# Kernel optimization log

Hardware: AMD Instinct MI355X
Metric: run time of the kernel (lower is better)

Reference implementation:

```python
import jax, jax.numpy as jnp
import numpy as np

B, S, D, H, FF, R = 4, 1024, 1024, 16, 4096, 128
DH = D // H


def rmsnorm(x, w, eps=1e-6):
    # matches torch: norm = ||x||_2 / sqrt(d); out = w * x / (norm + eps)
    n = jnp.sqrt(jnp.sum(x * x, axis=-1, keepdims=True)) / np.sqrt(x.shape[-1]).astype(np.float32)
    return w * x / (n + eps)


def setup_inputs() -> dict:
    key = jax.random.key(0)
    ks = jax.random.split(key, 20)
    def w(k, shape, s=0.02):
        return (jax.random.normal(k, shape, jnp.float32) * s)
    return {
        "x": jax.random.normal(ks[0], (B, S, D), jnp.float32),
        "norm1_w": jnp.ones((D,), jnp.float32),
        "Wq": w(ks[1], (D, D)), "bq": jnp.zeros((D,), jnp.float32),
        "Wk": w(ks[2], (D, D)), "bk": jnp.zeros((D,), jnp.float32),
        "Wv": w(ks[3], (D, D)), "bv": jnp.zeros((D,), jnp.float32),
        "Wz": w(ks[4], (D, D)), "bz": jnp.zeros((D,), jnp.float32),
        "Wg": w(ks[5], (D, D)), "bg": jnp.zeros((D,), jnp.float32),
        "gdw": w(ks[6], (R, D)), "gdb": jnp.zeros((R,), jnp.float32),
        "guw": w(ks[7], (D, R)), "gub": jnp.zeros((D,), jnp.float32),
        "Wo": w(ks[8], (D, D)), "bo": jnp.zeros((D,), jnp.float32),
        "norm2_w": jnp.ones((D,), jnp.float32),
        "f1w": w(ks[9], (FF, D)), "f1b": jnp.zeros((FF,), jnp.float32),
        "f2w": w(ks[10], (D, FF)), "f2b": jnp.zeros((D,), jnp.float32),
    }


def reference(x, norm1_w, Wq, bq, Wk, bk, Wv, bv, Wz, bz, Wg, bg,
              gdw, gdb, guw, gub, Wo, bo, norm2_w, f1w, f1b, f2w, f2b):
    b, s, d = x.shape
    h = d // DH
    # 1. Norm + Q/K/V/Z projections
    xn = rmsnorm(x, norm1_w)
    q = xn @ Wq.T + bq
    k = xn @ Wk.T + bk
    v = xn @ Wv.T + bv
    z = xn @ Wz.T + bz
    # 2-3. DPG decay: gamma_t = clamp(sigmoid(W_up ReLU(W_down z_t)))
    gamma = jax.nn.sigmoid(jax.nn.relu(z @ gdw.T + gdb) @ guw.T + gub)
    gamma = jnp.clip(gamma, 1e-6, 1.0 - 1e-6)
    # 4. Core recurrence: h_t = z_t * sigmoid(W_g h_{t-1}) + gamma_t * h_{t-1}
    def step(hprev, zg):
        zt, gt = zg
        hn = zt * jax.nn.sigmoid(hprev @ Wg.T + bg) + gt * hprev
        return hn, hn
    h0 = jnp.zeros((b, d), x.dtype)
    _, hs = jax.lax.scan(step, h0, (jnp.swapaxes(z, 0, 1), jnp.swapaxes(gamma, 0, 1)))
    hseq = jnp.swapaxes(hs, 0, 1)  # [B,S,D]
    # 5. Multi-head attention over Q,K,V
    qh = q.reshape(b, s, h, DH)
    kh = k.reshape(b, s, h, DH)
    vh = v.reshape(b, s, h, DH)
    scores = jnp.einsum('bqhd,bkhd->bhqk', qh, kh) / np.sqrt(DH).astype(np.float32)
    attn = jax.nn.softmax(scores, axis=-1)
    ao = jnp.einsum('bhqk,bkhd->bqhd', attn, vh).reshape(b, s, d)
    ao = ao @ Wo.T + bo
    # 6. Residuals
    y = x + ao + hseq
    # 7. FFN + output
    yn = rmsnorm(y, norm2_w)
    ff = jax.nn.gelu(yn @ f1w.T + f1b) @ f2w.T + f2b
    return y + ff
```

## Files before the change

### kernel.cpp

```cpp
#include <hip/hip_runtime.h>
#include <stdint.h>

#define DD 1024
#define SS 1024
#define NBS 32

typedef __attribute__((ext_vector_type(8))) __bf16 bf16x8;
typedef __attribute__((ext_vector_type(4))) float f32x4;

union Frag { uint4 u; bf16x8 b; };

__device__ __forceinline__ float bf2f(ushort u){ union{uint32_t i; float f;} c; c.i = ((uint32_t)u)<<16; return c.f; }
__device__ __forceinline__ float bflo(uint32_t p){ union{uint32_t i; float f;} c; c.i = p<<16; return c.f; }
__device__ __forceinline__ float bfhi(uint32_t p){ union{uint32_t i; float f;} c; c.i = p & 0xffff0000u; return c.f; }
__device__ __forceinline__ ushort f2bf(float f){
  union{float f; uint32_t u;} c; c.f = f;
  uint32_t u = c.u;
  return (ushort)((u + 0x7fffu + ((u>>16)&1u)) >> 16);
}

__global__ __launch_bounds__(256) void cast_k(const float* __restrict__ s,
    ushort* __restrict__ d, int n)
{
  int i = (blockIdx.x*256 + threadIdx.x)*4;
  if (i >= n) return;
  float4 v = *(const float4*)(s+i);
  ushort4 o; o.x=f2bf(v.x); o.y=f2bf(v.y); o.z=f2bf(v.z); o.w=f2bf(v.w);
  *(ushort4*)(d+i) = o;
}

__global__ __launch_bounds__(256) void rmsnorm_k(const float* __restrict__ X,
    const float* __restrict__ w, ushort* __restrict__ out)
{
  const int row = blockIdx.x, t = threadIdx.x;
  const float* x = X + (size_t)row*DD;
  float xs[4]; float s = 0.f;
  #pragma unroll
  for (int i=0;i<4;i++){ float v = x[t + i*256]; xs[i]=v; s += v*v; }
  #pragma unroll
  for (int off=32; off>0; off>>=1) s += __shfl_xor(s, off, 64);
  __shared__ float sred[4];
  if ((t&63)==0) sred[t>>6] = s;
  __syncthreads();
  s = sred[0]+sred[1]+sred[2]+sred[3];
  float inv = 1.f/(sqrtf(s)*0.03125f + 1e-6f);
  #pragma unroll
  for (int i=0;i<4;i++){
    int c2 = t + i*256;
    out[(size_t)row*DD + c2] = f2bf(xs[i]*inv*w[c2]);
  }
}

enum { ACT_NONE=0, ACT_RELU=1, ACT_SIG=2, ACT_GELU=3 };
enum { EPI_B16=0, EPI_DUAL=1, EPI_F32=2, EPI_Y=3, EPI_OUT=4 };

template<int ACT, int EPI>
__global__ __launch_bounds__(256) void gemm_bt(
    const ushort* __restrict__ A, const ushort* __restrict__ W,
    const float* __restrict__ bias, int N, int K,
    ushort* __restrict__ Ob, float* __restrict__ Of,
    const float* __restrict__ X32, const ushort* __restrict__ H16,
    const float* __restrict__ Yf)
{
  __shared__ __align__(16) ushort At[128*32];
  __shared__ __align__(16) ushort Wt[128*32];
  const int tid = threadIdx.x;
  const int wave = tid >> 6, lane = tid & 63;
  const int quad = lane >> 4, l16 = lane & 15;
  const int wr = wave >> 1, wc = wave & 1;
  const int m0 = blockIdx.x * 128, n0 = blockIdx.y * 128;

  f32x4 acc[4][4];
  const f32x4 vz = {0.f,0.f,0.f,0.f};
  #pragma unroll
  for (int i=0;i<4;i++)
    #pragma unroll
    for (int j=0;j<4;j++) acc[i][j] = vz;

  const ushort* gA = A + (size_t)(m0 + wave*32 + (lane>>2))*K + (lane&3)*8;
  const ushort* gW = W + (size_t)(n0 + wave*32 + (lane>>2))*K + (lane&3)*8;
  ushort* lA = At + wave*1024 + lane*8;
  ushort* lW = Wt + wave*1024 + lane*8;

  for (int ko = 0; ko < K; ko += 32) {
    uint4 va  = *(const uint4*)(gA + ko);
    uint4 va2 = *(const uint4*)(gA + ko + (size_t)16*K);
    uint4 vw  = *(const uint4*)(gW + ko);
    uint4 vw2 = *(const uint4*)(gW + ko + (size_t)16*K);
    __syncthreads();
    *(uint4*)lA          = va;
    *(uint4*)(lA + 512)  = va2;
    *(uint4*)lW          = vw;
    *(uint4*)(lW + 512)  = vw2;
    __syncthreads();
    Frag af[4], bfr[4];
    #pragma unroll
    for (int mi=0;mi<4;mi++)
      af[mi].u = *(const uint4*)&At[(wr*64 + mi*16 + l16)*32 + quad*8];
    #pragma unroll
    for (int ni=0;ni<4;ni++)
      bfr[ni].u = *(const uint4*)&Wt[(wc*64 + ni*16 + l16)*32 + quad*8];
    #pragma unroll
    for (int mi=0;mi<4;mi++)
      #pragma unroll
      for (int ni=0;ni<4;ni++)
        acc[mi][ni] = __builtin_amdgcn_mfma_f32_16x16x32_bf16(af[mi].b, bfr[ni].b, acc[mi][ni], 0,0,0);
  }

  float bia[4];
  #pragma unroll
  for (int ni=0;ni<4;ni++) bia[ni] = bias[n0 + wc*64 + ni*16 + l16];
  #pragma unroll
  for (int mi=0;mi<4;mi++) {
    const int row0 = m0 + wr*64 + mi*16 + quad*4;
    #pragma unroll
    for (int ni=0;ni<4;ni++) {
      const int col = n0 + wc*64 + ni*16 + l16;
      #pragma unroll
      for (int r=0;r<4;r++) {
        float vx = acc[mi][ni][r] + bia[ni];
        if (ACT == ACT_RELU) vx = fmaxf(vx, 0.f);
        else if (ACT == ACT_SIG) {
          vx = 1.f/(1.f+__expf(-vx));
          vx = fminf(fmaxf(vx, 1e-6f), 1.f-1e-6f);
        } else if (ACT == ACT_GELU) {
          float ci = 0.7978845608028654f*(vx + 0.044715f*vx*vx*vx);
          float th = 1.f - 2.f/(1.f + __expf(2.f*ci));
          vx = 0.5f*vx*(1.f+th);
        }
        size_t idx = (size_t)(row0 + r)*N + col;
        if (EPI == EPI_B16)      Ob[idx] = f2bf(vx);
        else if (EPI == EPI_DUAL){ Ob[idx] = f2bf(vx); Of[idx] = vx; }
        else if (EPI == EPI_F32)  Of[idx] = vx;
        else if (EPI == EPI_Y)    Of[idx] = vx + X32[idx] + bf2f(H16[idx]);
        else                      Of[idx] = vx + Yf[idx];
      }
    }
  }
}

__global__ __launch_bounds__(256) void attn_k(const ushort* __restrict__ q,
  const ushort* __restrict__ k, const ushort* __restrict__ v, ushort* __restrict__ ao)
{
  __shared__ __align__(16) ushort Ks[64*64];
  __shared__ __align__(16) ushort Vs[64*64];
  __shared__ float Ps[64*65];
  const int qt = blockIdx.x, bh = blockIdx.y;
  const int b = bh >> 4, h = bh & 15;
  const int t = threadIdx.x, r = t >> 2, seg = t & 3;
  const ushort* qrow = q + ((size_t)(b*SS + qt*64 + r))*DD + h*64;
  float qr[64];
  #pragma unroll
  for (int i=0;i<64;i+=8){
    uint4 u = *(const uint4*)(qrow + i);
    qr[i+0]=bflo(u.x); qr[i+1]=bfhi(u.x); qr[i+2]=bflo(u.y); qr[i+3]=bfhi(u.y);
    qr[i+4]=bflo(u.z); qr[i+5]=bfhi(u.z); qr[i+6]=bflo(u.w); qr[i+7]=bfhi(u.w);
  }
  float o[16];
  #pragma unroll
  for (int i=0;i<16;i++) o[i]=0.f;
  float mrun = -1e30f, lrun = 0.f;
  const int jrow = t >> 3, jch = t & 7;
  for (int kt=0; kt<16; kt++) {
    __syncthreads();
    const ushort* kg = k + ((size_t)(b*SS + kt*64))*DD + h*64;
    const ushort* vg = v + ((size_t)(b*SS + kt*64))*DD + h*64;
    #pragma unroll
    for (int part=0; part<2; part++){
      int j = jrow + part*32;
      *(uint4*)&Ks[j*64 + jch*8] = *(const uint4*)(kg + (size_t)j*DD + jch*8);
      *(uint4*)&Vs[j*64 + jch*8] = *(const uint4*)(vg + (size_t)j*DD + jch*8);
    }
    __syncthreads();
    float sc[16];
    #pragma unroll
    for (int jj=0;jj<16;jj++){
      int j = seg*16 + jj;
      float s_ = 0.f;
      #pragma unroll
      for (int i=0;i<64;i+=8){
        uint4 u = *(const uint4*)&Ks[j*64+i];
        s_ = fmaf(qr[i+0], bflo(u.x), s_); s_ = fmaf(qr[i+1], bfhi(u.x), s_);
        s_ = fmaf(qr[i+2], bflo(u.y), s_); s_ = fmaf(qr[i+3], bfhi(u.y), s_);
        s_ = fmaf(qr[i+4], bflo(u.z), s_); s_ = fmaf(qr[i+5], bfhi(u.z), s_);
        s_ = fmaf(qr[i+6], bflo(u.w), s_); s_ = fmaf(qr[i+7], bfhi(u.w), s_);
      }
      sc[jj] = s_ * 0.125f;
    }
    float mx = sc[0];
    #pragma unroll
    for (int jj=1;jj<16;jj++) mx = fmaxf(mx, sc[jj]);
    mx = fmaxf(mx, __shfl_xor(mx, 1, 64));
    mx = fmaxf(mx, __shfl_xor(mx, 2, 64));
    float mnew = fmaxf(mrun, mx);
    float psum = 0.f;
    #pragma unroll
    for (int jj=0;jj<16;jj++){
      float p = __expf(sc[jj]-mnew);
      Ps[r*65 + seg*16 + jj] = p;
      psum += p;
    }
    psum += __shfl_xor(psum, 1, 64);
    psum += __shfl_xor(psum, 2, 64);
    float alpha = __expf(mrun - mnew);
    lrun = lrun*alpha + psum;
    mrun = mnew;
    #pragma unroll
    for (int i=0;i<16;i++) o[i] *= alpha;
    __syncthreads();
    #pragma unroll 4
    for (int j=0;j<64;j++){
      float pj = Ps[r*65 + j];
      uint4 u0 = *(const uint4*)&Vs[j*64 + seg*16];
      uint4 u1 = *(const uint4*)&Vs[j*64 + seg*16 + 8];
      o[ 0]=fmaf(pj,bflo(u0.x),o[ 0]); o[ 1]=fmaf(pj,bfhi(u0.x),o[ 1]);
      o[ 2]=fmaf(pj,bflo(u0.y),o[ 2]); o[ 3]=fmaf(pj,bfhi(u0.y),o[ 3]);
      o[ 4]=fmaf(pj,bflo(u0.z),o[ 4]); o[ 5]=fmaf(pj,bfhi(u0.z),o[ 5]);
      o[ 6]=fmaf(pj,bflo(u0.w),o[ 6]); o[ 7]=fmaf(pj,bfhi(u0.w),o[ 7]);
      o[ 8]=fmaf(pj,bflo(u1.x),o[ 8]); o[ 9]=fmaf(pj,bfhi(u1.x),o[ 9]);
      o[10]=fmaf(pj,bflo(u1.y),o[10]); o[11]=fmaf(pj,bfhi(u1.y),o[11]);
      o[12]=fmaf(pj,bflo(u1.z),o[12]); o[13]=fmaf(pj,bfhi(u1.z),o[13]);
      o[14]=fmaf(pj,bflo(u1.w),o[14]); o[15]=fmaf(pj,bfhi(u1.w),o[15]);
    }
  }
  float invl = 1.f/lrun;
  ushort* orow = ao + ((size_t)(b*SS + qt*64 + r))*DD + h*64 + seg*16;
  #pragma unroll
  for (int i=0;i<16;i++) orow[i] = f2bf(o[i]*invl);
}

__global__ __launch_bounds__(256) void scan_k(
    const ushort* __restrict__ Wgb, const float* __restrict__ bg,
    const float* __restrict__ z32, const float* __restrict__ gm32,
    ushort* __restrict__ hseq, ushort* __restrict__ hstate)
{
  const int blk = blockIdx.x, t = threadIdx.x;
  const int wave = t>>6, lane = t&63, quad = lane>>4, c = lane&15;
  const int mt = wave & 1, kh = wave >> 1;
  const int nbase = blk*32 + mt*16;
  const bool epi = (kh == 0) && (c < 4);
  const int n0w = nbase + quad*4;
  Frag a[16];
  {
    const ushort* wrow = Wgb + (size_t)(nbase + c)*DD + kh*512 + quad*8;
    #pragma unroll
    for (int kt=0;kt<16;kt++) a[kt].u = *(const uint4*)(wrow + kt*32);
  }
  float bgv[4];
  #pragma unroll
  for (int r=0;r<4;r++) bgv[r] = bg[nbase + quad*4 + r];
  __shared__ __align__(16) ushort Hs[4096];
  __shared__ float redbuf[2][64][5];
  const int qi = (c*1024 + n0w) >> 2;
  int gmax = 256;

  float4 znx = {0,0,0,0}, gnx = {0,0,0,0};
  if (epi) {
    znx = *(const float4*)(z32  + ((size_t)c*SS + 0)*DD + n0w);
    gnx = *(const float4*)(gm32 + ((size_t)c*SS + 0)*DD + n0w);
  }

  for (int st=0; st<SS; st++) {
    if (st > 0) {
      const uint64_t* hrd = (const uint64_t*)(hstate + ((st+3)&3)*4096);
      uint64_t v0,v1,v2,v3;
      int guard = 0;
      for (;;) {
        v0 = __hip_atomic_load(hrd + t*4 + 0, __ATOMIC_RELAXED, __HIP_MEMORY_SCOPE_AGENT);
        v1 = __hip_atomic_load(hrd + t*4 + 1, __ATOMIC_RELAXED, __HIP_MEMORY_SCOPE_AGENT);
        v2 = __hip_atomic_load(hrd + t*4 + 2, __ATOMIC_RELAXED, __HIP_MEMORY_SCOPE_AGENT);
        v3 = __hip_atomic_load(hrd + t*4 + 3, __ATOMIC_RELAXED, __HIP_MEMORY_SCOPE_AGENT);
        bool ok = ((uint32_t)v0 != 0xFFFFFFFFu) & ((uint32_t)(v0>>32) != 0xFFFFFFFFu)
                & ((uint32_t)v1 != 0xFFFFFFFFu) & ((uint32_t)(v1>>32) != 0xFFFFFFFFu)
                & ((uint32_t)v2 != 0xFFFFFFFFu) & ((uint32_t)(v2>>32) != 0xFFFFFFFFu)
                & ((uint32_t)v3 != 0xFFFFFFFFu) & ((uint32_t)(v3>>32) != 0xFFFFFFFFu);
        if (ok) break;
        if (++guard > gmax) { gmax = 0; break; }
        __builtin_amdgcn_s_sleep(1);
      }
      if (epi) {
        uint64_t* rst = (uint64_t*)(hstate + ((st+2)&3)*4096);
        __hip_atomic_store(rst + qi, 0xFFFFFFFFFFFFFFFFull,
                           __ATOMIC_RELAXED, __HIP_MEMORY_SCOPE_AGENT);
      }
      uint64_t* hsd = (uint64_t*)Hs;
      hsd[t*4+0]=v0; hsd[t*4+1]=v1; hsd[t*4+2]=v2; hsd[t*4+3]=v3;
    }
    float4 zc = znx, gc = gnx;
    if (epi && (st+1 < SS)) {
      znx = *(const float4*)(z32  + ((size_t)c*SS + (st+1))*DD + n0w);
      gnx = *(const float4*)(gm32 + ((size_t)c*SS + (st+1))*DD + n0w);
    }
    if (st > 0) {
      asm volatile("s_waitcnt lgkmcnt(0)\ns_barrier" ::: "memory");
    }
    f32x4 acc = {0.f,0.f,0.f,0.f};
    if (st > 0) {
      f32x4 acc1 = {0.f,0.f,0.f,0.f};
      const uint4 z4 = make_uint4(0u,0u,0u,0u);
      #pragma unroll
      for (int kt=0;kt<16;kt+=2) {
        Frag b0, b1;
        b0.u = (c<4) ? *(const uint4*)&Hs[c*1024 + kh*512 + (kt  )*32 + quad*8] : z4;
        b1.u = (c<4) ? *(const uint4*)&Hs[c*1024 + kh*512 + (kt+1)*32 + quad*8] : z4;
        acc  = __builtin_amdgcn_mfma_f32_16x16x32_bf16(a[kt  ].b, b0.b, acc,  0,0,0);
        acc1 = __builtin_amdgcn_mfma_f32_16x16x32_bf16(a[kt+1].b, b1.b, acc1, 0,0,0);
      }
      #pragma unroll
      for (int r=0;r<4;r++) acc[r] += acc1[r];
    }
    if (kh == 1) {
      #pragma unroll
      for (int r=0;r<4;r++) redbuf[mt][lane][r] = acc[r];
    }
    asm volatile("s_waitcnt lgkmcnt(0)\ns_barrier" ::: "memory");
    if (epi) {
      ushort hb[4];
      float zr[4] = {zc.x, zc.y, zc.z, zc.w};
      float gr[4] = {gc.x, gc.y, gc.z, gc.w};
      #pragma unroll
      for (int r=0;r<4;r++) {
        float g = acc[r] + redbuf[mt][lane][r] + bgv[r];
        g = 1.f/(1.f+__expf(-g));
        float hp = (st>0) ? bf2f(Hs[c*1024 + n0w + r]) : 0.f;
        hb[r] = f2bf(zr[r]*g + gr[r]*hp);
      }
      uint32_t p0 = (uint32_t)hb[0] | ((uint32_t)hb[1]<<16);
      uint32_t p1 = (uint32_t)hb[2] | ((uint32_t)hb[3]<<16);
      uint64_t pk = ((uint64_t)p1<<32) | (uint64_t)p0;
      uint64_t* hwd = (uint64_t*)(hstate + (st&3)*4096);
      __hip_atomic_store(hwd + qi, pk, __ATOMIC_RELAXED, __HIP_MEMORY_SCOPE_AGENT);
      uint2* sq = (uint2*)(hseq + ((size_t)c*SS + st)*DD + n0w);
      *sq = make_uint2(p0, p1);
    }
    asm volatile("s_waitcnt lgkmcnt(0)\ns_barrier" ::: "memory");
  }
}

extern "C" void kernel_launch(void* const* d_in, const int* in_sizes, int n_in,
                              void* d_out, int out_size, void* d_ws, size_t ws_size,
                              hipStream_t stream)
{
  const float* x   = (const float*)d_in[0];
  const float* n1w = (const float*)d_in[1];
  const float* Wq  = (const float*)d_in[2];
  const float* bq  = (const float*)d_in[3];
  const float* Wk  = (const float*)d_in[4];
  const float* bk  = (const float*)d_in[5];
  const float* Wv  = (const float*)d_in[6];
  const float* bv  = (const float*)d_in[7];
  const float* Wz  = (const float*)d_in[8];
  const float* bz  = (const float*)d_in[9];
  const float* Wg_ = (const float*)d_in[10];
  const float* bg  = (const float*)d_in[11];
  const float* gdw = (const float*)d_in[12];
  const float* gdb = (const float*)d_in[13];
  const float* guw = (const float*)d_in[14];
  const float* gub = (const float*)d_in[15];
  const float* Wo  = (const float*)d_in[16];
  const float* bo  = (const float*)d_in[17];
  const float* n2w = (const float*)d_in[18];
  const float* f1w = (const float*)d_in[19];
  const float* f1b = (const float*)d_in[20];
  const float* f2w = (const float*)d_in[21];
  const float* f2b = (const float*)d_in[22];

  char* ws = (char*)d_ws;
  const size_t MB = (size_t)1<<20;
  ushort* Wqb  = (ushort*)(ws +  0*MB);
  ushort* Wkb  = (ushort*)(ws +  2*MB);
  ushort* Wvb  = (ushort*)(ws +  4*MB);
  ushort* Wzb  = (ushort*)(ws +  6*MB);
  ushort* Wob  = (ushort*)(ws +  8*MB);
  ushort* Wgb  = (ushort*)(ws + 10*MB);
  ushort* gdwb = (ushort*)(ws + 12*MB);
  ushort* guwb = (ushort*)(ws + 12*MB + (512<<10));
  ushort* f1wb = (ushort*)(ws + 13*MB);
  ushort* f2wb = (ushort*)(ws + 21*MB);
  ushort* xn   = (ushort*)(ws + 29*MB);
  ushort* qb   = (ushort*)(ws + 37*MB);
  ushort* kb   = (ushort*)(ws + 45*MB);
  ushort* vb   = (ushort*)(ws + 53*MB);
  ushort* zb16 = (ushort*)(ws + 61*MB);
  ushort* ff1  = (ushort*)(ws + 37*MB);
  ushort* t1   = (ushort*)(ws + 69*MB);
  ushort* hseq = (ushort*)(ws + 70*MB);
  ushort* aob  = (ushort*)(ws + 78*MB);
  float*  zb32 = (float*) (ws + 86*MB);
  float*  yf   = (float*) (ws + 86*MB);
  float*  gm32 = (float*) (ws +102*MB);
  ushort* hst  = (ushort*)(ws +118*MB);
  ushort* yn = xn;

  cast_k<<<1024, 256, 0, stream>>>(Wq,  Wqb, 1048576);
  cast_k<<<1024, 256, 0, stream>>>(Wk,  Wkb, 1048576);
  cast_k<<<1024, 256, 0, stream>>>(Wv,  Wvb, 1048576);
  cast_k<<<1024, 256, 0, stream>>>(Wz,  Wzb, 1048576);
  cast_k<<<1024, 256, 0, stream>>>(Wo,  Wob, 1048576);
  cast_k<<<1024, 256, 0, stream>>>(Wg_, Wgb, 1048576);
  cast_k<<< 128, 256, 0, stream>>>(gdw, gdwb, 131072);
  cast_k<<< 128, 256, 0, stream>>>(guw, guwb, 131072);
  cast_k<<<4096, 256, 0, stream>>>(f1w, f1wb, 4194304);
  cast_k<<<4096, 256, 0, stream>>>(f2w, f2wb, 4194304);
  rmsnorm_k<<<4096, 256, 0, stream>>>(x, n1w, xn);
  gemm_bt<ACT_NONE,EPI_B16 ><<<dim3(32,8), 256, 0, stream>>>(xn, Wqb, bq, 1024, 1024, qb,  nullptr, nullptr, nullptr, nullptr);
  gemm_bt<ACT_NONE,EPI_B16 ><<<dim3(32,8), 256, 0, stream>>>(xn, Wkb, bk, 1024, 1024, kb,  nullptr, nullptr, nullptr, nullptr);
  gemm_bt<ACT_NONE,EPI_B16 ><<<dim3(32,8), 256, 0, stream>>>(xn, Wvb, bv, 1024, 1024, vb,  nullptr, nullptr, nullptr, nullptr);
  gemm_bt<ACT_NONE,EPI_DUAL><<<dim3(32,8), 256, 0, stream>>>(xn, Wzb, bz, 1024, 1024, zb16, zb32,   nullptr, nullptr, nullptr);
  gemm_bt<ACT_RELU,EPI_B16><<<dim3(32,1), 256, 0, stream>>>(zb16, gdwb, gdb, 128, 1024, t1, nullptr, nullptr, nullptr, nullptr);
  gemm_bt<ACT_SIG ,EPI_F32><<<dim3(32,8), 256, 0, stream>>>(t1, guwb, gub, 1024, 128, nullptr, gm32, nullptr, nullptr, nullptr);
  attn_k<<<dim3(16,64), 256, 0, stream>>>(qb, kb, vb, aob);
  (void)hipMemsetAsync(hst, 0xFF, 32768, stream);
  scan_k<<<dim3(NBS), 256, 0, stream>>>(Wgb, bg, zb32, gm32, hseq, hst);
  gemm_bt<ACT_NONE,EPI_Y><<<dim3(32,8), 256, 0, stream>>>(aob, Wob, bo, 1024, 1024, nullptr, yf, x, hseq, nullptr);
  rmsnorm_k<<<4096, 256, 0, stream>>>(yf, n2w, yn);
  gemm_bt<ACT_GELU,EPI_B16><<<dim3(32,32), 256, 0, stream>>>(yn, f1wb, f1b, 4096, 1024, ff1, nullptr, nullptr, nullptr, nullptr);
  gemm_bt<ACT_NONE,EPI_OUT><<<dim3(32,8), 256, 0, stream>>>(ff1, f2wb, f2b, 1024, 4096, nullptr, (float*)d_out, nullptr, nullptr, yf);
}
```

Before: 4.927 ms.

## Restructure recurrence scan into 8 larger blocks with full-K waves and double-buffered state

The sequential scan kernel now runs as 8 blocks of 512 threads, each covering 128 output columns. Each wave holds the full 1024-wide slice of Wg in registers, so the split-K partial-sum reduction through shared memory goes away. The shared hidden-state buffer is double-buffered, which lets each timestep use one barrier instead of three. This cuts per-step synchronisation and cross-block polling overhead, but it doubles register usage per thread for the weight fragments and halves the per-wave parallelism across K.

```diff
diff --git a/kernel.cpp b/kernel.cpp
--- a/kernel.cpp
+++ b/kernel.cpp
@@ -3,7 +3,7 @@
 
 #define DD 1024
 #define SS 1024
-#define NBS 32
+#define NBS 8
 
 typedef __attribute__((ext_vector_type(8))) __bf16 bf16x8;
 typedef __attribute__((ext_vector_type(4))) float f32x4;
@@ -229,28 +229,28 @@
   for (int i=0;i<16;i++) orow[i] = f2bf(o[i]*invl);
 }
 
-__global__ __launch_bounds__(256) void scan_k(
+__global__ __launch_bounds__(512, 2) void scan_k(
     const ushort* __restrict__ Wgb, const float* __restrict__ bg,
     const float* __restrict__ z32, const float* __restrict__ gm32,
     ushort* __restrict__ hseq, ushort* __restrict__ hstate)
 {
   const int blk = blockIdx.x, t = threadIdx.x;
   const int wave = t>>6, lane = t&63, quad = lane>>4, c = lane&15;
-  const int mt = wave & 1, kh = wave >> 1;
-  const int nbase = blk*32 + mt*16;
-  const bool epi = (kh == 0) && (c < 4);
+  const int nbase = blk*128 + wave*16;
   const int n0w = nbase + quad*4;
-  Frag a[16];
+  const bool epi = (c < 4);
+  Frag a[32];
   {
-    const ushort* wrow = Wgb + (size_t)(nbase + c)*DD + kh*512 + quad*8;
-    #pragma unroll
-    for (int kt=0;kt<16;kt++) a[kt].u = *(const uint4*)(wrow + kt*32);
+    const ushort* wrow = Wgb + (size_t)(nbase + c)*DD + quad*8;
+    #pragma unroll
+    for (int kt=0;kt<32;kt++) a[kt].u = *(const uint4*)(wrow + kt*32);
   }
   float bgv[4];
-  #pragma unroll
-  for (int r=0;r<4;r++) bgv[r] = bg[nbase + quad*4 + r];
-  __shared__ __align__(16) ushort Hs[4096];
-  __shared__ float redbuf[2][64][5];
+  {
+    float4 b4 = *(const float4*)(bg + n0w);
+    bgv[0]=b4.x; bgv[1]=b4.y; bgv[2]=b4.z; bgv[3]=b4.w;
+  }
+  __shared__ __align__(16) ushort Hs[2][4096];
   const int qi = (c*1024 + n0w) >> 2;
   int gmax = 256;
 
@@ -261,19 +261,16 @@
   }
 
   for (int st=0; st<SS; st++) {
+    const int cur = st & 1;
     if (st > 0) {
-      const uint64_t* hrd = (const uint64_t*)(hstate + ((st+3)&3)*4096);
-      uint64_t v0,v1,v2,v3;
+      const uint64_t* hrd = (const uint64_t*)(hstate + ((st+3)&3)*4096) + t*2;
+      uint64_t v0,v1;
       int guard = 0;
       for (;;) {
-        v0 = __hip_atomic_load(hrd + t*4 + 0, __ATOMIC_RELAXED, __HIP_MEMORY_SCOPE_AGENT);
-        v1 = __hip_atomic_load(hrd + t*4 + 1, __ATOMIC_RELAXED, __HIP_MEMORY_SCOPE_AGENT);
-        v2 = __hip_atomic_load(hrd + t*4 + 2, __ATOMIC_RELAXED, __HIP_MEMORY_SCOPE_AGENT);
-        v3 = __hip_atomic_load(hrd + t*4 + 3, __ATOMIC_RELAXED, __HIP_MEMORY_SCOPE_AGENT);
+        v0 = __hip_atomic_load(hrd + 0, __ATOMIC_RELAXED, __HIP_MEMORY_SCOPE_AGENT);
+        v1 = __hip_atomic_load(hrd + 1, __ATOMIC_RELAXED, __HIP_MEMORY_SCOPE_AGENT);
         bool ok = ((uint32_t)v0 != 0xFFFFFFFFu) & ((uint32_t)(v0>>32) != 0xFFFFFFFFu)
-                & ((uint32_t)v1 != 0xFFFFFFFFu) & ((uint32_t)(v1>>32) != 0xFFFFFFFFu)
-                & ((uint32_t)v2 != 0xFFFFFFFFu) & ((uint32_t)(v2>>32) != 0xFFFFFFFFu)
-                & ((uint32_t)v3 != 0xFFFFFFFFu) & ((uint32_t)(v3>>32) != 0xFFFFFFFFu);
+                & ((uint32_t)v1 != 0xFFFFFFFFu) & ((uint32_t)(v1>>32) != 0xFFFFFFFFu);
         if (ok) break;
         if (++guard > gmax) { gmax = 0; break; }
         __builtin_amdgcn_s_sleep(1);
@@ -283,46 +280,40 @@
         __hip_atomic_store(rst + qi, 0xFFFFFFFFFFFFFFFFull,
                            __ATOMIC_RELAXED, __HIP_MEMORY_SCOPE_AGENT);
       }
-      uint64_t* hsd = (uint64_t*)Hs;
-      hsd[t*4+0]=v0; hsd[t*4+1]=v1; hsd[t*4+2]=v2; hsd[t*4+3]=v3;
+      uint64_t* hsd = (uint64_t*)Hs[cur];
+      hsd[t*2  ] = v0;
+      hsd[t*2+1] = v1;
     }
     float4 zc = znx, gc = gnx;
     if (epi && (st+1 < SS)) {
       znx = *(const float4*)(z32  + ((size_t)c*SS + (st+1))*DD + n0w);
       gnx = *(const float4*)(gm32 + ((size_t)c*SS + (st+1))*DD + n0w);
     }
-    if (st > 0) {
-      asm volatile("s_waitcnt lgkmcnt(0)\ns_barrier" ::: "memory");
-    }
+    asm volatile("s_waitcnt lgkmcnt(0)\ns_barrier" ::: "memory");
     f32x4 acc = {0.f,0.f,0.f,0.f};
     if (st > 0) {
       f32x4 acc1 = {0.f,0.f,0.f,0.f};
       const uint4 z4 = make_uint4(0u,0u,0u,0u);
       #pragma unroll
-      for (int kt=0;kt<16;kt+=2) {
+      for (int kt=0;kt<32;kt+=2) {
         Frag b0, b1;
-        b0.u = (c<4) ? *(const uint4*)&Hs[c*1024 + kh*512 + (kt  )*32 + quad*8] : z4;
-        b1.u = (c<4) ? *(const uint4*)&Hs[c*1024 + kh*512 + (kt+1)*32 + quad*8] : z4;
+        b0.u = (c<4) ? *(const uint4*)&Hs[cur][c*1024 + (kt  )*32 + quad*8] : z4;
+        b1.u = (c<4) ? *(const uint4*)&Hs[cur][c*1024 + (kt+1)*32 + quad*8] : z4;
         acc  = __builtin_amdgcn_mfma_f32_16x16x32_bf16(a[kt  ].b, b0.b, acc,  0,0,0);
         acc1 = __builtin_amdgcn_mfma_f32_16x16x32_bf16(a[kt+1].b, b1.b, acc1, 0,0,0);
       }
       #pragma unroll
       for (int r=0;r<4;r++) acc[r] += acc1[r];
     }
-    if (kh == 1) {
-      #pragma unroll
-      for (int r=0;r<4;r++) redbuf[mt][lane][r] = acc[r];
-    }
-    asm volatile("s_waitcnt lgkmcnt(0)\ns_barrier" ::: "memory");
     if (epi) {
       ushort hb[4];
       float zr[4] = {zc.x, zc.y, zc.z, zc.w};
       float gr[4] = {gc.x, gc.y, gc.z, gc.w};
       #pragma unroll
       for (int r=0;r<4;r++) {
-        float g = acc[r] + redbuf[mt][lane][r] + bgv[r];
+        float g = acc[r] + bgv[r];
         g = 1.f/(1.f+__expf(-g));
-        float hp = (st>0) ? bf2f(Hs[c*1024 + n0w + r]) : 0.f;
+        float hp = (st>0) ? bf2f(Hs[cur][c*1024 + n0w + r]) : 0.f;
         hb[r] = f2bf(zr[r]*g + gr[r]*hp);
       }
       uint32_t p0 = (uint32_t)hb[0] | ((uint32_t)hb[1]<<16);
@@ -333,7 +324,6 @@
       uint2* sq = (uint2*)(hseq + ((size_t)c*SS + st)*DD + n0w);
       *sq = make_uint2(p0, p1);
     }
-    asm volatile("s_waitcnt lgkmcnt(0)\ns_barrier" ::: "memory");
   }
 }
 
@@ -411,7 +401,7 @@
   gemm_bt<ACT_SIG ,EPI_F32><<<dim3(32,8), 256, 0, stream>>>(t1, guwb, gub, 1024, 128, nullptr, gm32, nullptr, nullptr, nullptr);
   attn_k<<<dim3(16,64), 256, 0, stream>>>(qb, kb, vb, aob);
   (void)hipMemsetAsync(hst, 0xFF, 32768, stream);
-  scan_k<<<dim3(NBS), 256, 0, stream>>>(Wgb, bg, zb32, gm32, hseq, hst);
+  scan_k<<<dim3(NBS), 512, 0, stream>>>(Wgb, bg, zb32, gm32, hseq, hst);
   gemm_bt<ACT_NONE,EPI_Y><<<dim3(32,8), 256, 0, stream>>>(aob, Wob, bo, 1024, 1024, nullptr, yf, x, hseq, nullptr);
   rmsnorm_k<<<4096, 256, 0, stream>>>(yf, n2w, yn);
   gemm_bt<ACT_GELU,EPI_B16><<<dim3(32,32), 256, 0, stream>>>(yn, f1wb, f1b, 4096, 1024, ff1, nullptr, nullptr, nullptr, nullptr);
```

New measurement: 8.671 ms. 1.76x slower.

## Fuse scan, attention and late weight casts into one concurrent kernel

Applied to the files above, without the earlier changes.

The sequential recurrence scan (32 blocks), the attention kernel and the Wo/f1w/f2w bf16 casts now run as one launch, with block ID ranges selecting each role. The scan keeps only 32 CUs busy for 1024 serial steps, so the idea is to fill the idle CUs with attention and cast work instead of running them in separate launches. Shared memory is unified into a single byte buffer. The scan's cross-block spin-waits assume all 32 scan blocks are resident at once; they have the lowest IDs and so are likely scheduled first, but they now share CUs with co-resident attention blocks, which may slow each scan step.

```diff
diff --git a/kernel.cpp b/kernel.cpp
--- a/kernel.cpp
+++ b/kernel.cpp
@@ -139,201 +139,226 @@
   }
 }
 
-__global__ __launch_bounds__(256) void attn_k(const ushort* __restrict__ q,
-  const ushort* __restrict__ k, const ushort* __restrict__ v, ushort* __restrict__ ao)
-{
-  __shared__ __align__(16) ushort Ks[64*64];
-  __shared__ __align__(16) ushort Vs[64*64];
-  __shared__ float Ps[64*65];
-  const int qt = blockIdx.x, bh = blockIdx.y;
-  const int b = bh >> 4, h = bh & 15;
-  const int t = threadIdx.x, r = t >> 2, seg = t & 3;
-  const ushort* qrow = q + ((size_t)(b*SS + qt*64 + r))*DD + h*64;
-  float qr[64];
-  #pragma unroll
-  for (int i=0;i<64;i+=8){
-    uint4 u = *(const uint4*)(qrow + i);
-    qr[i+0]=bflo(u.x); qr[i+1]=bfhi(u.x); qr[i+2]=bflo(u.y); qr[i+3]=bfhi(u.y);
-    qr[i+4]=bflo(u.z); qr[i+5]=bfhi(u.z); qr[i+6]=bflo(u.w); qr[i+7]=bfhi(u.w);
-  }
-  float o[16];
-  #pragma unroll
-  for (int i=0;i<16;i++) o[i]=0.f;
-  float mrun = -1e30f, lrun = 0.f;
-  const int jrow = t >> 3, jch = t & 7;
-  for (int kt=0; kt<16; kt++) {
-    __syncthreads();
-    const ushort* kg = k + ((size_t)(b*SS + kt*64))*DD + h*64;
-    const ushort* vg = v + ((size_t)(b*SS + kt*64))*DD + h*64;
-    #pragma unroll
-    for (int part=0; part<2; part++){
-      int j = jrow + part*32;
-      *(uint4*)&Ks[j*64 + jch*8] = *(const uint4*)(kg + (size_t)j*DD + jch*8);
-      *(uint4*)&Vs[j*64 + jch*8] = *(const uint4*)(vg + (size_t)j*DD + jch*8);
-    }
-    __syncthreads();
-    float sc[16];
-    #pragma unroll
-    for (int jj=0;jj<16;jj++){
-      int j = seg*16 + jj;
-      float s_ = 0.f;
-      #pragma unroll
-      for (int i=0;i<64;i+=8){
-        uint4 u = *(const uint4*)&Ks[j*64+i];
-        s_ = fmaf(qr[i+0], bflo(u.x), s_); s_ = fmaf(qr[i+1], bfhi(u.x), s_);
-        s_ = fmaf(qr[i+2], bflo(u.y), s_); s_ = fmaf(qr[i+3], bfhi(u.y), s_);
-        s_ = fmaf(qr[i+4], bflo(u.z), s_); s_ = fmaf(qr[i+5], bfhi(u.z), s_);
-        s_ = fmaf(qr[i+6], bflo(u.w), s_); s_ = fmaf(qr[i+7], bfhi(u.w), s_);
-      }
-      sc[jj] = s_ * 0.125f;
-    }
-    float mx = sc[0];
-    #pragma unroll
-    for (int jj=1;jj<16;jj++) mx = fmaxf(mx, sc[jj]);
-    mx = fmaxf(mx, __shfl_xor(mx, 1, 64));
-    mx = fmaxf(mx, __shfl_xor(mx, 2, 64));
-    float mnew = fmaxf(mrun, mx);
-    float psum = 0.f;
-    #pragma unroll
-    for (int jj=0;jj<16;jj++){
-      float p = __expf(sc[jj]-mnew);
-      Ps[r*65 + seg*16 + jj] = p;
-      psum += p;
-    }
-    psum += __shfl_xor(psum, 1, 64);
-    psum += __shfl_xor(psum, 2, 64);
-    float alpha = __expf(mrun - mnew);
-    lrun = lrun*alpha + psum;
-    mrun = mnew;
-    #pragma unroll
-    for (int i=0;i<16;i++) o[i] *= alpha;
-    __syncthreads();
-    #pragma unroll 4
-    for (int j=0;j<64;j++){
-      float pj = Ps[r*65 + j];
-      uint4 u0 = *(const uint4*)&Vs[j*64 + seg*16];
-      uint4 u1 = *(const uint4*)&Vs[j*64 + seg*16 + 8];
-      o[ 0]=fmaf(pj,bflo(u0.x),o[ 0]); o[ 1]=fmaf(pj,bfhi(u0.x),o[ 1]);
-      o[ 2]=fmaf(pj,bflo(u0.y),o[ 2]); o[ 3]=fmaf(pj,bfhi(u0.y),o[ 3]);
-      o[ 4]=fmaf(pj,bflo(u0.z),o[ 4]); o[ 5]=fmaf(pj,bfhi(u0.z),o[ 5]);
-      o[ 6]=fmaf(pj,bflo(u0.w),o[ 6]); o[ 7]=fmaf(pj,bfhi(u0.w),o[ 7]);
-      o[ 8]=fmaf(pj,bflo(u1.x),o[ 8]); o[ 9]=fmaf(pj,bfhi(u1.x),o[ 9]);
-      o[10]=fmaf(pj,bflo(u1.y),o[10]); o[11]=fmaf(pj,bfhi(u1.y),o[11]);
-      o[12]=fmaf(pj,bflo(u1.z),o[12]); o[13]=fmaf(pj,bfhi(u1.z),o[13]);
-      o[14]=fmaf(pj,bflo(u1.w),o[14]); o[15]=fmaf(pj,bfhi(u1.w),o[15]);
-    }
-  }
-  float invl = 1.f/lrun;
-  ushort* orow = ao + ((size_t)(b*SS + qt*64 + r))*DD + h*64 + seg*16;
-  #pragma unroll
-  for (int i=0;i<16;i++) orow[i] = f2bf(o[i]*invl);
-}
-
-__global__ __launch_bounds__(256) void scan_k(
+__global__ __launch_bounds__(256) void fused_k(
     const ushort* __restrict__ Wgb, const float* __restrict__ bg,
     const float* __restrict__ z32, const float* __restrict__ gm32,
-    ushort* __restrict__ hseq, ushort* __restrict__ hstate)
+    ushort* __restrict__ hseq, ushort* __restrict__ hstate,
+    const ushort* __restrict__ q, const ushort* __restrict__ k,
+    const ushort* __restrict__ v, ushort* __restrict__ ao,
+    const float* __restrict__ Wo32, ushort* __restrict__ Wob,
+    const float* __restrict__ f1w32, ushort* __restrict__ f1wb,
+    const float* __restrict__ f2w32, ushort* __restrict__ f2wb)
 {
-  const int blk = blockIdx.x, t = threadIdx.x;
-  const int wave = t>>6, lane = t&63, quad = lane>>4, c = lane&15;
-  const int mt = wave & 1, kh = wave >> 1;
-  const int nbase = blk*32 + mt*16;
-  const bool epi = (kh == 0) && (c < 4);
-  const int n0w = nbase + quad*4;
-  Frag a[16];
+  __shared__ __align__(16) char smem[33024];
+  const int bid0 = blockIdx.x;
+  const int t = threadIdx.x;
+
+  if (bid0 < 32) {
+    const int blk = bid0;
+    const int wave = t>>6, lane = t&63, quad = lane>>4, c = lane&15;
+    const int mt = wave & 1, kh = wave >> 1;
+    const int nbase = blk*32 + mt*16;
+    const bool epi = (kh == 0) && (c < 4);
+    const int n0w = nbase + quad*4;
+    Frag a[16];
+    {
+      const ushort* wrow = Wgb + (size_t)(nbase + c)*DD + kh*512 + quad*8;
+      #pragma unroll
+      for (int kt=0;kt<16;kt++) a[kt].u = *(const uint4*)(wrow + kt*32);
+    }
+    float bgv[4];
+    #pragma unroll
+    for (int r=0;r<4;r++) bgv[r] = bg[nbase + quad*4 + r];
+    ushort* Hs = (ushort*)smem;
+    float*  redbuf = (float*)(smem + 8192);
+    const int qi = (c*1024 + n0w) >> 2;
+    int gmax = 256;
+
+    float4 znx = {0,0,0,0}, gnx = {0,0,0,0};
+    if (epi) {
+      znx = *(const float4*)(z32  + ((size_t)c*SS + 0)*DD + n0w);
+      gnx = *(const float4*)(gm32 + ((size_t)c*SS + 0)*DD + n0w);
+    }
+
+    for (int st=0; st<SS; st++) {
+      if (st > 0) {
+        const uint64_t* hrd = (const uint64_t*)(hstate + ((st+3)&3)*4096);
+        uint64_t v0,v1,v2,v3;
+        int guard = 0;
+        for (;;) {
+          v0 = __hip_atomic_load(hrd + t*4 + 0, __ATOMIC_RELAXED, __HIP_MEMORY_SCOPE_AGENT);
+          v1 = __hip_atomic_load(hrd + t*4 + 1, __ATOMIC_RELAXED, __HIP_MEMORY_SCOPE_AGENT);
+          v2 = __hip_atomic_load(hrd + t*4 + 2, __ATOMIC_RELAXED, __HIP_MEMORY_SCOPE_AGENT);
+          v3 = __hip_atomic_load(hrd + t*4 + 3, __ATOMIC_RELAXED, __HIP_MEMORY_SCOPE_AGENT);
+          bool ok = ((uint32_t)v0 != 0xFFFFFFFFu) & ((uint32_t)(v0>>32) != 0xFFFFFFFFu)
+                  & ((uint32_t)v1 != 0xFFFFFFFFu) & ((uint32_t)(v1>>32) != 0xFFFFFFFFu)
+                  & ((uint32_t)v2 != 0xFFFFFFFFu) & ((uint32_t)(v2>>32) != 0xFFFFFFFFu)
+                  & ((uint32_t)v3 != 0xFFFFFFFFu) & ((uint32_t)(v3>>32) != 0xFFFFFFFFu);
+          if (ok) break;
+          if (++guard > gmax) { gmax = 0; break; }
+          __builtin_amdgcn_s_sleep(1);
+        }
+        if (epi) {
+          uint64_t* rst = (uint64_t*)(hstate + ((st+2)&3)*4096);
+          __hip_atomic_store(rst + qi, 0xFFFFFFFFFFFFFFFFull,
+                             __ATOMIC_RELAXED, __HIP_MEMORY_SCOPE_AGENT);
+        }
+        uint64_t* hsd = (uint64_t*)Hs;
+        hsd[t*4+0]=v0; hsd[t*4+1]=v1; hsd[t*4+2]=v2; hsd[t*4+3]=v3;
+      }
+      float4 zc = znx, gc = gnx;
+      if (epi && (st+1 < SS)) {
+        znx = *(const float4*)(z32  + ((size_t)c*SS + (st+1))*DD + n0w);
+        gnx = *(const float4*)(gm32 + ((size_t)c*SS + (st+1))*DD + n0w);
+      }
+      if (st > 0) {
+        asm volatile("s_waitcnt lgkmcnt(0)\ns_barrier" ::: "memory");
+      }
+      f32x4 acc = {0.f,0.f,0.f,0.f};
+      if (st > 0) {
+        f32x4 acc1 = {0.f,0.f,0.f,0.f};
+        const uint4 z4 = make_uint4(0u,0u,0u,0u);
+        #pragma unroll
+        for (int kt=0;kt<16;kt+=2) {
+          Frag b0, b1;
+          b0.u = (c<4) ? *(const uint4*)&Hs[c*1024 + kh*512 + (kt  )*32 + quad*8] : z4;
+          b1.u = (c<4) ? *(const uint4*)&Hs[c*1024 + kh*512 + (kt+1)*32 + quad*8] : z4;
+          acc  = __builtin_amdgcn_mfma_f32_16x16x32_bf16(a[kt  ].b, b0.b, acc,  0,0,0);
+          acc1 = __builtin_amdgcn_mfma_f32_16x16x32_bf16(a[kt+1].b, b1.b, acc1, 0,0,0);
+        }
+        #pragma unroll
+        for (int r=0;r<4;r++) acc[r] += acc1[r];
+      }
+      if (kh == 1) {
+        #pragma unroll
+        for (int r=0;r<4;r++) redbuf[(mt*64 + lane)*5 + r] = acc[r];
+      }
+      asm volatile("s_waitcnt lgkmcnt(0)\ns_barrier" ::: "memory");
+      if (epi) {
+        ushort hb[4];
+        float zr[4] = {zc.x, zc.y, zc.z, zc.w};
+        float gr[4] = {gc.x, gc.y, gc.z, gc.w};
+        #pragma unroll
+        for (int r=0;r<4;r++) {
+          float g = acc[r] + redbuf[(mt*64 + lane)*5 + r] + bgv[r];
+          g = 1.f/(1.f+__expf(-g));
+          float hp = (st>0) ? bf2f(Hs[c*1024 + n0w + r]) : 0.f;
+          hb[r] = f2bf(zr[r]*g + gr[r]*hp);
+        }
+        uint32_t p0 = (uint32_t)hb[0] | ((uint32_t)hb[1]<<16);
+        uint32_t p1 = (uint32_t)hb[2] | ((uint32_t)hb[3]<<16);
+        uint64_t pk = ((uint64_t)p1<<32) | (uint64_t)p0;
+        uint64_t* hwd = (uint64_t*)(hstate + (st&3)*4096);
+        __hip_atomic_store(hwd + qi, pk, __ATOMIC_RELAXED, __HIP_MEMORY_SCOPE_AGENT);
+        uint2* sq = (uint2*)(hseq + ((size_t)c*SS + st)*DD + n0w);
+        *sq = make_uint2(p0, p1);
+      }
+      asm volatile("s_waitcnt lgkmcnt(0)\ns_barrier" ::: "memory");
+    }
+    return;
+  }
+
+  if (bid0 < 1056) {
+    const int abid = bid0 - 32;
+    const int qt = abid & 15, bh = abid >> 4;
+    const int b = bh >> 4, h = bh & 15;
+    const int r = t >> 2, seg = t & 3;
+    ushort* Ks = (ushort*)smem;
+    ushort* Vs = (ushort*)(smem + 8192);
+    float*  Ps = (float*)(smem + 16384);
+    const ushort* qrow = q + ((size_t)(b*SS + qt*64 + r))*DD + h*64;
+    float qr[64];
+    #pragma unroll
+    for (int i=0;i<64;i+=8){
+      uint4 u = *(const uint4*)(qrow + i);
+      qr[i+0]=bflo(u.x); qr[i+1]=bfhi(u.x); qr[i+2]=bflo(u.y); qr[i+3]=bfhi(u.y);
+      qr[i+4]=bflo(u.z); qr[i+5]=bfhi(u.z); qr[i+6]=bflo(u.w); qr[i+7]=bfhi(u.w);
+    }
+    float o[16];
+    #pragma unroll
+    for (int i=0;i<16;i++) o[i]=0.f;
+    float mrun = -1e30f, lrun = 0.f;
+    const int jrow = t >> 3, jch = t & 7;
+    for (int kt=0; kt<16; kt++) {
+      __syncthreads();
+      const ushort* kg = k + ((size_t)(b*SS + kt*64))*DD + h*64;
+      const ushort* vg = v + ((size_t)(b*SS + kt*64))*DD + h*64;
+      #pragma unroll
+      for (int part=0; part<2; part++){
+        int j = jrow + part*32;
+        *(uint4*)&Ks[j*64 + jch*8] = *(const uint4*)(kg + (size_t)j*DD + jch*8);
+        *(uint4*)&Vs[j*64 + jch*8] = *(const uint4*)(vg + (size_t)j*DD + jch*8);
+      }
+      __syncthreads();
+      float sc[16];
+      #pragma unroll
+      for (int jj=0;jj<16;jj++){
+        int j = seg*16 + jj;
+        float s_ = 0.f;
+        #pragma unroll
+        for (int i=0;i<64;i+=8){
+          uint4 u = *(const uint4*)&Ks[j*64+i];
+          s_ = fmaf(qr[i+0], bflo(u.x), s_); s_ = fmaf(qr[i+1], bfhi(u.x), s_);
+          s_ = fmaf(qr[i+2], bflo(u.y), s_); s_ = fmaf(qr[i+3], bfhi(u.y), s_);
+          s_ = fmaf(qr[i+4], bflo(u.z), s_); s_ = fmaf(qr[i+5], bfhi(u.z), s_);
+          s_ = fmaf(qr[i+6], bflo(u.w), s_); s_ = fmaf(qr[i+7], bfhi(u.w), s_);
+        }
+        sc[jj] = s_ * 0.125f;
+      }
+      float mx = sc[0];
+      #pragma unroll
+      for (int jj=1;jj<16;jj++) mx = fmaxf(mx, sc[jj]);
+      mx = fmaxf(mx, __shfl_xor(mx, 1, 64));
+      mx = fmaxf(mx, __shfl_xor(mx, 2, 64));
+      float mnew = fmaxf(mrun, mx);
+      float psum = 0.f;
+      #pragma unroll
+      for (int jj=0;jj<16;jj++){
+        float p = __expf(sc[jj]-mnew);
+        Ps[r*65 + seg*16 + jj] = p;
+        psum += p;
+      }
+      psum += __shfl_xor(psum, 1, 64);
+      psum += __shfl_xor(psum, 2, 64);
+      float alpha = __expf(mrun - mnew);
+      lrun = lrun*alpha + psum;
+      mrun = mnew;
+      #pragma unroll
+      for (int i=0;i<16;i++) o[i] *= alpha;
+      __syncthreads();
+      #pragma unroll 4
+      for (int j=0;j<64;j++){
+        float pj = Ps[r*65 + j];
+        uint4 u0 = *(const uint4*)&Vs[j*64 + seg*16];
+        uint4 u1 = *(const uint4*)&Vs[j*64 + seg*16 + 8];
+        o[ 0]=fmaf(pj,bflo(u0.x),o[ 0]); o[ 1]=fmaf(pj,bfhi(u0.x),o[ 1]);
+        o[ 2]=fmaf(pj,bflo(u0.y),o[ 2]); o[ 3]=fmaf(pj,bfhi(u0.y),o[ 3]);
+        o[ 4]=fmaf(pj,bflo(u0.z),o[ 4]); o[ 5]=fmaf(pj,bfhi(u0.z),o[ 5]);
+        o[ 6]=fmaf(pj,bflo(u0.w),o[ 6]); o[ 7]=fmaf(pj,bfhi(u0.w),o[ 7]);
+        o[ 8]=fmaf(pj,bflo(u1.x),o[ 8]); o[ 9]=fmaf(pj,bfhi(u1.x),o[ 9]);
+        o[10]=fmaf(pj,bflo(u1.y),o[10]); o[11]=fmaf(pj,bfhi(u1.y),o[11]);
+        o[12]=fmaf(pj,bflo(u1.z),o[12]); o[13]=fmaf(pj,bfhi(u1.z),o[13]);
+        o[14]=fmaf(pj,bflo(u1.w),o[14]); o[15]=fmaf(pj,bfhi(u1.w),o[15]);
+      }
+    }
+    float invl = 1.f/lrun;
+    ushort* orow = ao + ((size_t)(b*SS + qt*64 + r))*DD + h*64 + seg*16;
+    #pragma unroll
+    for (int i=0;i<16;i++) orow[i] = f2bf(o[i]*invl);
+    return;
+  }
+
   {
-    const ushort* wrow = Wgb + (size_t)(nbase + c)*DD + kh*512 + quad*8;
-    #pragma unroll
-    for (int kt=0;kt<16;kt++) a[kt].u = *(const uint4*)(wrow + kt*32);
-  }
-  float bgv[4];
-  #pragma unroll
-  for (int r=0;r<4;r++) bgv[r] = bg[nbase + quad*4 + r];
-  __shared__ __align__(16) ushort Hs[4096];
-  __shared__ float redbuf[2][64][5];
-  const int qi = (c*1024 + n0w) >> 2;
-  int gmax = 256;
-
-  float4 znx = {0,0,0,0}, gnx = {0,0,0,0};
-  if (epi) {
-    znx = *(const float4*)(z32  + ((size_t)c*SS + 0)*DD + n0w);
-    gnx = *(const float4*)(gm32 + ((size_t)c*SS + 0)*DD + n0w);
-  }
-
-  for (int st=0; st<SS; st++) {
-    if (st > 0) {
-      const uint64_t* hrd = (const uint64_t*)(hstate + ((st+3)&3)*4096);
-      uint64_t v0,v1,v2,v3;
-      int guard = 0;
-      for (;;) {
-        v0 = __hip_atomic_load(hrd + t*4 + 0, __ATOMIC_RELAXED, __HIP_MEMORY_SCOPE_AGENT);
-        v1 = __hip_atomic_load(hrd + t*4 + 1, __ATOMIC_RELAXED, __HIP_MEMORY_SCOPE_AGENT);
-        v2 = __hip_atomic_load(hrd + t*4 + 2, __ATOMIC_RELAXED, __HIP_MEMORY_SCOPE_AGENT);
-        v3 = __hip_atomic_load(hrd + t*4 + 3, __ATOMIC_RELAXED, __HIP_MEMORY_SCOPE_AGENT);
-        bool ok = ((uint32_t)v0 != 0xFFFFFFFFu) & ((uint32_t)(v0>>32) != 0xFFFFFFFFu)
-                & ((uint32_t)v1 != 0xFFFFFFFFu) & ((uint32_t)(v1>>32) != 0xFFFFFFFFu)
-                & ((uint32_t)v2 != 0xFFFFFFFFu) & ((uint32_t)(v2>>32) != 0xFFFFFFFFu)
-                & ((uint32_t)v3 != 0xFFFFFFFFu) & ((uint32_t)(v3>>32) != 0xFFFFFFFFu);
-        if (ok) break;
-        if (++guard > gmax) { gmax = 0; break; }
-        __builtin_amdgcn_s_sleep(1);
-      }
-      if (epi) {
-        uint64_t* rst = (uint64_t*)(hstate + ((st+2)&3)*4096);
-        __hip_atomic_store(rst + qi, 0xFFFFFFFFFFFFFFFFull,
-                           __ATOMIC_RELAXED, __HIP_MEMORY_SCOPE_AGENT);
-      }
-      uint64_t* hsd = (uint64_t*)Hs;
-      hsd[t*4+0]=v0; hsd[t*4+1]=v1; hsd[t*4+2]=v2; hsd[t*4+3]=v3;
-    }
-    float4 zc = znx, gc = gnx;
-    if (epi && (st+1 < SS)) {
-      znx = *(const float4*)(z32  + ((size_t)c*SS + (st+1))*DD + n0w);
-      gnx = *(const float4*)(gm32 + ((size_t)c*SS + (st+1))*DD + n0w);
-    }
-    if (st > 0) {
-      asm volatile("s_waitcnt lgkmcnt(0)\ns_barrier" ::: "memory");
-    }
-    f32x4 acc = {0.f,0.f,0.f,0.f};
-    if (st > 0) {
-      f32x4 acc1 = {0.f,0.f,0.f,0.f};
-      const uint4 z4 = make_uint4(0u,0u,0u,0u);
-      #pragma unroll
-      for (int kt=0;kt<16;kt+=2) {
-        Frag b0, b1;
-        b0.u = (c<4) ? *(const uint4*)&Hs[c*1024 + kh*512 + (kt  )*32 + quad*8] : z4;
-        b1.u = (c<4) ? *(const uint4*)&Hs[c*1024 + kh*512 + (kt+1)*32 + quad*8] : z4;
-        acc  = __builtin_amdgcn_mfma_f32_16x16x32_bf16(a[kt  ].b, b0.b, acc,  0,0,0);
-        acc1 = __builtin_amdgcn_mfma_f32_16x16x32_bf16(a[kt+1].b, b1.b, acc1, 0,0,0);
-      }
-      #pragma unroll
-      for (int r=0;r<4;r++) acc[r] += acc1[r];
-    }
-    if (kh == 1) {
-      #pragma unroll
-      for (int r=0;r<4;r++) redbuf[mt][lane][r] = acc[r];
-    }
-    asm volatile("s_waitcnt lgkmcnt(0)\ns_barrier" ::: "memory");
-    if (epi) {
-      ushort hb[4];
-      float zr[4] = {zc.x, zc.y, zc.z, zc.w};
-      float gr[4] = {gc.x, gc.y, gc.z, gc.w};
-      #pragma unroll
-      for (int r=0;r<4;r++) {
-        float g = acc[r] + redbuf[mt][lane][r] + bgv[r];
-        g = 1.f/(1.f+__expf(-g));
-        float hp = (st>0) ? bf2f(Hs[c*1024 + n0w + r]) : 0.f;
-        hb[r] = f2bf(zr[r]*g + gr[r]*hp);
-      }
-      uint32_t p0 = (uint32_t)hb[0] | ((uint32_t)hb[1]<<16);
-      uint32_t p1 = (uint32_t)hb[2] | ((uint32_t)hb[3]<<16);
-      uint64_t pk = ((uint64_t)p1<<32) | (uint64_t)p0;
-      uint64_t* hwd = (uint64_t*)(hstate + (st&3)*4096);
-      __hip_atomic_store(hwd + qi, pk, __ATOMIC_RELAXED, __HIP_MEMORY_SCOPE_AGENT);
-      uint2* sq = (uint2*)(hseq + ((size_t)c*SS + st)*DD + n0w);
-      *sq = make_uint2(p0, p1);
-    }
-    asm volatile("s_waitcnt lgkmcnt(0)\ns_barrier" ::: "memory");
+    int cbid = bid0 - 1056;
+    const float* src; ushort* dst; int n;
+    if (cbid < 1024)      { src = Wo32;  dst = Wob;  n = 1048576; }
+    else if (cbid < 5120) { src = f1w32; dst = f1wb; n = 4194304; cbid -= 1024; }
+    else                  { src = f2w32; dst = f2wb; n = 4194304; cbid -= 5120; }
+    int i = (cbid*256 + t)*4;
+    if (i >= n) return;
+    float4 vv = *(const float4*)(src+i);
+    ushort4 oo; oo.x=f2bf(vv.x); oo.y=f2bf(vv.y); oo.z=f2bf(vv.z); oo.w=f2bf(vv.w);
+    *(ushort4*)(dst+i) = oo;
   }
 }
 
@@ -396,12 +421,9 @@
   cast_k<<<1024, 256, 0, stream>>>(Wk,  Wkb, 1048576);
   cast_k<<<1024, 256, 0, stream>>>(Wv,  Wvb, 1048576);
   cast_k<<<1024, 256, 0, stream>>>(Wz,  Wzb, 1048576);
-  cast_k<<<1024, 256, 0, stream>>>(Wo,  Wob, 1048576);
   cast_k<<<1024, 256, 0, stream>>>(Wg_, Wgb, 1048576);
   cast_k<<< 128, 256, 0, stream>>>(gdw, gdwb, 131072);
   cast_k<<< 128, 256, 0, stream>>>(guw, guwb, 131072);
-  cast_k<<<4096, 256, 0, stream>>>(f1w, f1wb, 4194304);
-  cast_k<<<4096, 256, 0, stream>>>(f2w, f2wb, 4194304);
   rmsnorm_k<<<4096, 256, 0, stream>>>(x, n1w, xn);
   gemm_bt<ACT_NONE,EPI_B16 ><<<dim3(32,8), 256, 0, stream>>>(xn, Wqb, bq, 1024, 1024, qb,  nullptr, nullptr, nullptr, nullptr);
   gemm_bt<ACT_NONE,EPI_B16 ><<<dim3(32,8), 256, 0, stream>>>(xn, Wkb, bk, 1024, 1024, kb,  nullptr, nullptr, nullptr, nullptr);
@@ -409,9 +431,10 @@
   gemm_bt<ACT_NONE,EPI_DUAL><<<dim3(32,8), 256, 0, stream>>>(xn, Wzb, bz, 1024, 1024, zb16, zb32,   nullptr, nullptr, nullptr);
   gemm_bt<ACT_RELU,EPI_B16><<<dim3(32,1), 256, 0, stream>>>(zb16, gdwb, gdb, 128, 1024, t1, nullptr, nullptr, nullptr, nullptr);
   gemm_bt<ACT_SIG ,EPI_F32><<<dim3(32,8), 256, 0, stream>>>(t1, guwb, gub, 1024, 128, nullptr, gm32, nullptr, nullptr, nullptr);
-  attn_k<<<dim3(16,64), 256, 0, stream>>>(qb, kb, vb, aob);
   (void)hipMemsetAsync(hst, 0xFF, 32768, stream);
-  scan_k<<<dim3(NBS), 256, 0, stream>>>(Wgb, bg, zb32, gm32, hseq, hst);
+  fused_k<<<dim3(10272), 256, 0, stream>>>(Wgb, bg, zb32, gm32, hseq, hst,
+                                           qb, kb, vb, aob,
+                                           Wo, Wob, f1w, f1wb, f2w, f2wb);
   gemm_bt<ACT_NONE,EPI_Y><<<dim3(32,8), 256, 0, stream>>>(aob, Wob, bo, 1024, 1024, nullptr, yf, x, hseq, nullptr);
   rmsnorm_k<<<4096, 256, 0, stream>>>(yf, n2w, yn);
   gemm_bt<ACT_GELU,EPI_B16><<<dim3(32,32), 256, 0, stream>>>(yn, f1wb, f1b, 4096, 1024, ff1, nullptr, nullptr, nullptr, nullptr);
```

Measured after the change: 4.440 ms. -9.9%, faster.
